# Optimization experiments

Measured on AMD Instinct MI355X. Metric: run time of the kernel, lower is better.

## Reference

```python
import jax, jax.numpy as jnp
import numpy as np

NUM_NODES = 100000
NUM_EDGES = 3200000
NUM_GRAPHS = 64


def gcn_conv(x, edge_index, W, b):
    """PyG GCNConv: add self-loops, symmetric deg normalization, linear, scatter-add."""
    n = x.shape[0]
    loop = jnp.arange(n, dtype=edge_index.dtype)
    src = jnp.concatenate([edge_index[0], loop])  # message sources
    dst = jnp.concatenate([edge_index[1], loop])  # aggregation targets
    deg = jax.ops.segment_sum(jnp.ones_like(src, dtype=x.dtype), dst, num_segments=n)
    dis = jnp.where(deg > 0, jax.lax.rsqrt(jnp.maximum(deg, 1.0)), 0.0)
    norm = dis[src] * dis[dst]  # [E+N]
    h = x @ W  # linear transform first (small dims)
    msg = h[src] * norm[:, None]  # irregular gather
    out = jax.ops.segment_sum(msg, dst, num_segments=n)  # scatter-add
    return out + b


def setup_inputs() -> dict:
    key = jax.random.key(0)
    ks = jax.random.split(key, 12)
    x = jax.random.normal(ks[0], (NUM_NODES, 3), dtype=jnp.float32)
    edge_index = jax.random.randint(ks[1], (2, NUM_EDGES), 0, NUM_NODES, dtype=jnp.int64)
    batch = jnp.sort(jax.random.randint(ks[2], (NUM_NODES,), 0, NUM_GRAPHS, dtype=jnp.int64))
    def glorot(k, fan_in, fan_out):
        s = (6.0 / (fan_in + fan_out)) ** 0.5
        return jax.random.uniform(k, (fan_in, fan_out), jnp.float32, -s, s)
    return {
        'x': x, 'edge_index': edge_index, 'batch': batch,
        'W1': glorot(ks[3], 3, 32), 'b1': jnp.zeros((32,), jnp.float32),
        'W2': glorot(ks[4], 32, 16), 'b2': jnp.zeros((16,), jnp.float32),
        'W3': glorot(ks[5], 16, 8), 'b3': jnp.zeros((8,), jnp.float32),
        'Wf': glorot(ks[6], 8, 3), 'bf': jnp.zeros((3,), jnp.float32),
    }


def reference(x, edge_index, batch, W1, b1, W2, b2, W3, b3, Wf, bf):
    h = jax.nn.relu(gcn_conv(x, edge_index, W1, b1))
    h = jax.nn.relu(gcn_conv(h, edge_index, W2, b2))
    h = jax.nn.relu(gcn_conv(h, edge_index, W3, b3))
    # global mean pool over graphs
    sums = jax.ops.segment_sum(h, batch, num_segments=NUM_GRAPHS)
    cnts = jax.ops.segment_sum(jnp.ones((h.shape[0],), h.dtype), batch, num_segments=NUM_GRAPHS)
    pooled = sums / jnp.maximum(cnts, 1.0)[:, None]
    return pooled @ Wf + bf
```

## Files before the change

### kernel.cpp

```cpp
#include <hip/hip_runtime.h>

constexpr int N_NODES  = 100000;
constexpr int N_EDGES  = 3200000;
constexpr int N_GRAPHS = 64;

constexpr int BSHIFT   = 8;
constexpr int NBINS    = (N_NODES + 255) >> BSHIFT;
constexpr int BIN_CAP  = 9216;
constexpr int SRC_BITS = 17;
constexpr int SRC_MASK = (1 << SRC_BITS) - 1;

constexpr int NB_BIN = 500;
constexpr int EPB    = N_EDGES / NB_BIN;
constexpr int EPT    = (EPB + 1023) / 1024;

typedef float v4f __attribute__((ext_vector_type(4)));


__global__ __launch_bounds__(1024) void bin_kernel(
        const int* __restrict__ src, const int* __restrict__ dst,
        int* __restrict__ bin_cur, int* __restrict__ binned) {
    __shared__ int pk[EPB];
    __shared__ unsigned short bn[EPB];
    __shared__ unsigned short ord[EPB];
    __shared__ int hist[NBINS];
    __shared__ int lexcl[NBINS];
    __shared__ int lofs[NBINS];
    __shared__ int gofs[NBINS];
    __shared__ int s512[512];
    int tid = threadIdx.x;
    int e0 = blockIdx.x * EPB;
    for (int i = tid; i < NBINS; i += 1024) hist[i] = 0;
    __syncthreads();
#pragma unroll
    for (int k = 0; k < EPT; ++k) {
        int i = tid + k * 1024;
        if (i < EPB) {
            int d = __builtin_nontemporal_load(&dst[e0 + i]);
            int s = __builtin_nontemporal_load(&src[e0 + i]);
            int b = d >> BSHIFT;
            pk[i] = ((d & 255) << SRC_BITS) | s;
            bn[i] = (unsigned short)b;
            atomicAdd(&hist[b], 1);
        }
    }
    __syncthreads();
    if (tid < 512) s512[tid] = (tid < NBINS) ? hist[tid] : 0;
    __syncthreads();
    for (int o = 1; o < 512; o <<= 1) {
        int x = 0;
        if (tid < 512 && tid >= o) x = s512[tid - o];
        __syncthreads();
        if (tid < 512) s512[tid] += x;
        __syncthreads();
    }
    if (tid < NBINS) {
        int h = hist[tid];
        int excl = s512[tid] - h;
        lexcl[tid] = excl;
        lofs[tid]  = excl;
        gofs[tid]  = h ? atomicAdd(&bin_cur[tid], h) : 0;
    }
    __syncthreads();
#pragma unroll
    for (int k = 0; k < EPT; ++k) {
        int i = tid + k * 1024;
        if (i < EPB) {
            int r = atomicAdd(&lofs[bn[i]], 1);
            ord[r] = (unsigned short)i;
        }
    }
    __syncthreads();
#pragma unroll
    for (int k = 0; k < EPT; ++k) {
        int i = tid + k * 1024;
        if (i < EPB) {
            int j = ord[i];
            int b = bn[j];
            int pos = gofs[b] + (i - lexcl[b]);
            if (pos < BIN_CAP)
                __builtin_nontemporal_store(pk[j], &binned[(size_t)b * BIN_CAP + pos]);
        }
    }
}

__global__ void binscan_kernel(const int* __restrict__ bin_cur, int* __restrict__ bin_base,
                               int* __restrict__ rowptr) {
    __shared__ int s[512];
    int t = threadIdx.x;
    int v = (t < NBINS) ? bin_cur[t] : 0;
    s[t] = v;
    __syncthreads();
    for (int o = 1; o < 512; o <<= 1) {
        int x = (t >= o) ? s[t - o] : 0;
        __syncthreads();
        s[t] += x;
        __syncthreads();
    }
    if (t < NBINS) bin_base[t] = s[t] - v;
    if (t == 0) rowptr[N_NODES] = N_EDGES;
}

__global__ __launch_bounds__(1024) void csrbuild_kernel(
        const int* __restrict__ binned, const int* __restrict__ bin_cur,
        const int* __restrict__ bin_base, int* __restrict__ rowptr,
        float* __restrict__ dis, int* __restrict__ csr) {
    __shared__ int cnt[256];
    __shared__ int lofs[256];
    __shared__ int s[256];
    int b = blockIdx.x;
    int t = threadIdx.x;
    int size  = min(bin_cur[b], BIN_CAP);
    int gbase = bin_base[b];
    const int* bp = binned + (size_t)b * BIN_CAP;
    if (t < 256) cnt[t] = 0;
    __syncthreads();
    int pc[9];
#pragma unroll
    for (int k = 0; k < 9; ++k) {
        int i = t + k * 1024;
        pc[k] = (i < size) ? __builtin_nontemporal_load(&bp[i]) : -1;
        if (i < size) atomicAdd(&cnt[pc[k] >> SRC_BITS], 1);
    }
    __syncthreads();
    if (t < 256) {
        int n = (b << BSHIFT) + t;
        int deg = cnt[t];
        if (n < N_NODES) dis[n] = 1.0f / sqrtf((float)deg + 1.0f);
        s[t] = deg;
    }
    __syncthreads();
    for (int o = 1; o < 256; o <<= 1) {
        int x = 0;
        if (t < 256 && t >= o) x = s[t - o];
        __syncthreads();
        if (t < 256) s[t] += x;
        __syncthreads();
    }
    if (t < 256) {
        int n = (b << BSHIFT) + t;
        int excl = s[t] - cnt[t];
        if (n < N_NODES) rowptr[n] = gbase + excl;
        lofs[t] = excl;
        cnt[t] = 0;
    }
    __syncthreads();
#pragma unroll
    for (int k = 0; k < 9; ++k) {
        int i = t + k * 1024;
        if (i < size) {
            int p = pc[k];
            int ln = p >> SRC_BITS;
            int r = atomicAdd(&cnt[ln], 1);
            csr[gbase + lofs[ln] + r] = p & SRC_MASK;
        }
    }
}


__global__ void pre1_kernel(const float* __restrict__ x, const float* __restrict__ dis,
                            float* __restrict__ xs) {
    int i = blockIdx.x * blockDim.x + threadIdx.x;
    if (i >= N_NODES) return;
    float d = dis[i];
    float4 v;
    v.x = __builtin_nontemporal_load(&x[(size_t)i * 3 + 0]) * d;
    v.y = __builtin_nontemporal_load(&x[(size_t)i * 3 + 1]) * d;
    v.z = __builtin_nontemporal_load(&x[(size_t)i * 3 + 2]) * d;
    v.w = 0.f;
    *reinterpret_cast<float4*>(&xs[(size_t)i * 4]) = v;
}

template<int F, bool ADD_B, bool RELU>
__global__ __launch_bounds__(256) void gather_kernel(
        const float* __restrict__ in, const int* __restrict__ rowptr,
        const int* __restrict__ csr, const float* __restrict__ dis,
        const float* __restrict__ b, float* __restrict__ out) {
    constexpr int VPL = F / 4;
    constexpr int NPB = 256 / 16;
    int tid  = threadIdx.x;
    int sub  = tid & 3;
    int qtr  = (tid >> 2) & 3;
    int n    = blockIdx.x * NPB + (tid >> 4);
    if (n >= N_NODES) return;
    int beg = rowptr[n], end = rowptr[n + 1];
    int len = end - beg;
    int kb = beg + ((len * qtr) >> 2);
    int ke = beg + ((len * (qtr + 1)) >> 2);
    const float* ip = in + (size_t)sub * VPL;
    float a0[VPL], a1[VPL], a2[VPL], a3[VPL];
#pragma unroll
    for (int j = 0; j < VPL; ++j) { a0[j] = 0.f; a1[j] = 0.f; a2[j] = 0.f; a3[j] = 0.f; }
    if (qtr == 0) {
#pragma unroll
        for (int j = 0; j < VPL; ++j) a0[j] = ip[(size_t)n * F + j];
    }
    int k = kb;
    for (; k + 7 < ke; k += 8) {
        int s0 = __builtin_nontemporal_load(&csr[k + 0]);
        int s1 = __builtin_nontemporal_load(&csr[k + 1]);
        int s2 = __builtin_nontemporal_load(&csr[k + 2]);
        int s3 = __builtin_nontemporal_load(&csr[k + 3]);
        int s4 = __builtin_nontemporal_load(&csr[k + 4]);
        int s5 = __builtin_nontemporal_load(&csr[k + 5]);
        int s6 = __builtin_nontemporal_load(&csr[k + 6]);
        int s7 = __builtin_nontemporal_load(&csr[k + 7]);
        const float* r0 = &ip[(size_t)s0 * F];
        const float* r1 = &ip[(size_t)s1 * F];
        const float* r2 = &ip[(size_t)s2 * F];
        const float* r3 = &ip[(size_t)s3 * F];
        const float* r4 = &ip[(size_t)s4 * F];
        const float* r5 = &ip[(size_t)s5 * F];
        const float* r6 = &ip[(size_t)s6 * F];
        const float* r7 = &ip[(size_t)s7 * F];
#pragma unroll
        for (int j = 0; j < VPL; ++j) a0[j] += r0[j];
#pragma unroll
        for (int j = 0; j < VPL; ++j) a1[j] += r1[j];
#pragma unroll
        for (int j = 0; j < VPL; ++j) a2[j] += r2[j];
#pragma unroll
        for (int j = 0; j < VPL; ++j) a3[j] += r3[j];
#pragma unroll
        for (int j = 0; j < VPL; ++j) a0[j] += r4[j];
#pragma unroll
        for (int j = 0; j < VPL; ++j) a1[j] += r5[j];
#pragma unroll
        for (int j = 0; j < VPL; ++j) a2[j] += r6[j];
#pragma unroll
        for (int j = 0; j < VPL; ++j) a3[j] += r7[j];
    }
    if (k + 3 < ke) {
        int s0 = __builtin_nontemporal_load(&csr[k + 0]);
        int s1 = __builtin_nontemporal_load(&csr[k + 1]);
        int s2 = __builtin_nontemporal_load(&csr[k + 2]);
        int s3 = __builtin_nontemporal_load(&csr[k + 3]);
        const float* r0 = &ip[(size_t)s0 * F];
        const float* r1 = &ip[(size_t)s1 * F];
        const float* r2 = &ip[(size_t)s2 * F];
        const float* r3 = &ip[(size_t)s3 * F];
#pragma unroll
        for (int j = 0; j < VPL; ++j) a0[j] += r0[j];
#pragma unroll
        for (int j = 0; j < VPL; ++j) a1[j] += r1[j];
#pragma unroll
        for (int j = 0; j < VPL; ++j) a2[j] += r2[j];
#pragma unroll
        for (int j = 0; j < VPL; ++j) a3[j] += r3[j];
        k += 4;
    }
    for (; k < ke; ++k) {
        int s0 = __builtin_nontemporal_load(&csr[k]);
        const float* r0 = &ip[(size_t)s0 * F];
#pragma unroll
        for (int j = 0; j < VPL; ++j) a0[j] += r0[j];
    }
    float v[VPL];
#pragma unroll
    for (int j = 0; j < VPL; ++j) v[j] = (a0[j] + a1[j]) + (a2[j] + a3[j]);
#pragma unroll
    for (int j = 0; j < VPL; ++j) v[j] += __shfl_xor(v[j], 4);
#pragma unroll
    for (int j = 0; j < VPL; ++j) v[j] += __shfl_xor(v[j], 8);
    if (qtr == 0) {
        float d = dis[n];
#pragma unroll
        for (int j = 0; j < VPL; ++j) {
            float w = v[j] * d;
            if (ADD_B) w += b[sub * VPL + j];
            if (RELU) w = fmaxf(w, 0.f);
            __builtin_nontemporal_store(w, &out[(size_t)n * F + sub * VPL + j]);
        }
    }
}

__global__ void lin1_kernel(const float* __restrict__ m, const float* __restrict__ W1,
                            const float* __restrict__ b1, float* __restrict__ h1) {
    int i = blockIdx.x * blockDim.x + threadIdx.x;
    if (i >= N_NODES) return;
    float4 mv = *reinterpret_cast<const float4*>(&m[(size_t)i * 4]);
#pragma unroll
    for (int f = 0; f < 32; ++f) {
        float s = b1[f];
        s = fmaf(mv.x, W1[0 * 32 + f], s);
        s = fmaf(mv.y, W1[1 * 32 + f], s);
        s = fmaf(mv.z, W1[2 * 32 + f], s);
        h1[(size_t)i * 32 + f] = fmaxf(s, 0.f);
    }
}

template<int FIN, int FOUT>
__global__ void lin_pre_kernel(const float* __restrict__ in, const float* __restrict__ W,
                               const float* __restrict__ dis, float* __restrict__ g) {
    int i = blockIdx.x * blockDim.x + threadIdx.x;
    if (i >= N_NODES) return;
    float xin[FIN];
    const v4f* hp = reinterpret_cast<const v4f*>(&in[(size_t)i * FIN]);
#pragma unroll
    for (int q = 0; q < FIN / 4; ++q) {
        v4f v = __builtin_nontemporal_load(&hp[q]);
        xin[q * 4 + 0] = v.x; xin[q * 4 + 1] = v.y;
        xin[q * 4 + 2] = v.z; xin[q * 4 + 3] = v.w;
    }
    float d = dis[i];
#pragma unroll
    for (int f = 0; f < FOUT; ++f) {
        float s = 0.f;
#pragma unroll
        for (int k = 0; k < FIN; ++k) s = fmaf(xin[k], W[k * FOUT + f], s);
        g[(size_t)i * FOUT + f] = s * d;
    }
}


__global__ void pool_kernel(const float* __restrict__ h, const int* __restrict__ batch,
                            float* __restrict__ pool) {
    __shared__ float lsum[N_GRAPHS * 8];
    __shared__ float lcnt[N_GRAPHS];
    int tid = threadIdx.x;
    for (int j = tid; j < N_GRAPHS * 8; j += blockDim.x) lsum[j] = 0.f;
    for (int j = tid; j < N_GRAPHS; j += blockDim.x) lcnt[j] = 0.f;
    __syncthreads();
    int i = blockIdx.x * blockDim.x + tid;
    if (i < N_NODES) {
        int gm = batch[i];
        const float4* hp = reinterpret_cast<const float4*>(&h[(size_t)i * 8]);
        float4 a = hp[0], bq = hp[1];
        atomicAdd(&lsum[gm * 8 + 0], a.x);
        atomicAdd(&lsum[gm * 8 + 1], a.y);
        atomicAdd(&lsum[gm * 8 + 2], a.z);
        atomicAdd(&lsum[gm * 8 + 3], a.w);
        atomicAdd(&lsum[gm * 8 + 4], bq.x);
        atomicAdd(&lsum[gm * 8 + 5], bq.y);
        atomicAdd(&lsum[gm * 8 + 6], bq.z);
        atomicAdd(&lsum[gm * 8 + 7], bq.w);
        atomicAdd(&lcnt[gm], 1.0f);
    }
    __syncthreads();
    for (int idx = tid; idx < N_GRAPHS * 9; idx += blockDim.x) {
        int gm = idx / 9, j = idx % 9;
        if (lcnt[gm] != 0.f) {
            if (j < 8) atomicAdd(&pool[gm * 8 + j], lsum[gm * 8 + j]);
            else       atomicAdd(&pool[512 + gm], lcnt[gm]);
        }
    }
}

__global__ void final_kernel(const float* __restrict__ pool, const float* __restrict__ Wf,
                             const float* __restrict__ bf, float* __restrict__ out) {
    int t = threadIdx.x;
    if (t >= N_GRAPHS * 3) return;
    int gm = t / 3, c = t % 3;
    float cnt = fmaxf(pool[512 + gm], 1.0f);
    float s = 0.f;
#pragma unroll
    for (int f = 0; f < 8; ++f) s = fmaf(pool[gm * 8 + f] / cnt, Wf[f * 3 + c], s);
    out[t] = s + bf[c];
}


extern "C" void kernel_launch(void* const* d_in, const int* in_sizes, int n_in,
                              void* d_out, int out_size, void* d_ws, size_t ws_size,
                              hipStream_t stream) {
    const float* x     = (const float*)d_in[0];
    const int*   ei    = (const int*)d_in[1];
    const int*   batch = (const int*)d_in[2];
    const float* W1 = (const float*)d_in[3];
    const float* b1 = (const float*)d_in[4];
    const float* W2 = (const float*)d_in[5];
    const float* b2 = (const float*)d_in[6];
    const float* W3 = (const float*)d_in[7];
    const float* b3 = (const float*)d_in[8];
    const float* Wf = (const float*)d_in[9];
    const float* bf = (const float*)d_in[10];

    const int* src = ei;
    const int* dst = ei + N_EDGES;

    const int N = N_NODES, E = N_EDGES;

    int*   bin_cur  = (int*)d_ws;
    int*   bin_base = bin_cur + NBINS;
    int*   rowptr   = bin_base + NBINS;
    float* dis      = (float*)(rowptr + N + 2);
    int*   csr      = (int*)(dis + N);
    float* act      = (float*)(csr + E);
    int*   binned   = (int*)act;
    float* xs   = act;
    float* m    = act + (size_t)4  * N;
    float* h1   = act + (size_t)8  * N;
    float* g    = act + (size_t)40 * N;
    float* h2   = act + (size_t)56 * N;
    float* pool = act + (size_t)72 * N;
    float* g8   = act;
    float* h3   = act + (size_t)8 * N;

    const int B = 256;
    const int NB_N = (N + B - 1) / B;
    const int NB_G = N / 16;

    hipMemsetAsync(bin_cur, 0, NBINS * sizeof(int), stream);
    hipMemsetAsync(pool, 0, N_GRAPHS * 9 * sizeof(float), stream);

    bin_kernel<<<NB_BIN, 1024, 0, stream>>>(src, dst, bin_cur, binned);
    binscan_kernel<<<1, 512, 0, stream>>>(bin_cur, bin_base, rowptr);
    csrbuild_kernel<<<NBINS, 1024, 0, stream>>>(binned, bin_cur, bin_base, rowptr, dis, csr);

    pre1_kernel<<<NB_N, B, 0, stream>>>(x, dis, xs);
    gather_kernel<4, false, false><<<NB_G, B, 0, stream>>>(xs, rowptr, csr, dis, b1, m);
    lin1_kernel<<<NB_N, B, 0, stream>>>(m, W1, b1, h1);

    lin_pre_kernel<32, 16><<<NB_N, B, 0, stream>>>(h1, W2, dis, g);
    gather_kernel<16, true, true><<<NB_G, B, 0, stream>>>(g, rowptr, csr, dis, b2, h2);

    lin_pre_kernel<16, 8><<<NB_N, B, 0, stream>>>(h2, W3, dis, g8);
    gather_kernel<8, true, true><<<NB_G, B, 0, stream>>>(g8, rowptr, csr, dis, b3, h3);

    pool_kernel<<<NB_N, B, 0, stream>>>(h3, batch, pool);
    final_kernel<<<1, 256, 0, stream>>>(pool, Wf, bf, (float*)d_out);
}
```

Baseline: 199.5 us.

## Fuse linear layers into gathers and pooling; split CSR rows by source half

Fuses lin1 with the W2 transform into one kernel, fuses the layer-2 gather with bias, ReLU and the W3 projection, and fuses the layer-3 gather with mean-pool accumulation. This removes three kernel launches and the round trips of the h1, h2 and h3 intermediates through global memory. The CSR build now sorts each row's edges into two halves by source index (below and above 50000) and records a rowmid pointer. The layer-2 gather walks the two halves separately, likely to improve cache locality of the gathered rows. The cost is extra shuffles, a larger scan in csrbuild, and more register pressure in the fused kernels.

```diff
diff --git a/kernel.cpp b/kernel.cpp
--- a/kernel.cpp
+++ b/kernel.cpp
@@ -3,6 +3,7 @@
 constexpr int N_NODES  = 100000;
 constexpr int N_EDGES  = 3200000;
 constexpr int N_GRAPHS = 64;
+constexpr int HALF_N   = 50000;
 
 constexpr int BSHIFT   = 8;
 constexpr int NBINS    = (N_NODES + 255) >> BSHIFT;
@@ -104,97 +105,70 @@
 __global__ __launch_bounds__(1024) void csrbuild_kernel(
         const int* __restrict__ binned, const int* __restrict__ bin_cur,
         const int* __restrict__ bin_base, int* __restrict__ rowptr,
-        float* __restrict__ dis, int* __restrict__ csr) {
-    __shared__ int cnt[256];
-    __shared__ int lofs[256];
-    __shared__ int s[256];
+        int* __restrict__ rowmid, float* __restrict__ dis, int* __restrict__ csr) {
+    __shared__ int cnt[512];
+    __shared__ int lofs[512];
+    __shared__ int s[512];
     int b = blockIdx.x;
     int t = threadIdx.x;
     int size  = min(bin_cur[b], BIN_CAP);
     int gbase = bin_base[b];
     const int* bp = binned + (size_t)b * BIN_CAP;
-    if (t < 256) cnt[t] = 0;
+    if (t < 512) cnt[t] = 0;
     __syncthreads();
     int pc[9];
 #pragma unroll
     for (int k = 0; k < 9; ++k) {
         int i = t + k * 1024;
         pc[k] = (i < size) ? __builtin_nontemporal_load(&bp[i]) : -1;
-        if (i < size) atomicAdd(&cnt[pc[k] >> SRC_BITS], 1);
-    }
+        if (i < size) {
+            int p = pc[k];
+            int idx = ((p >> SRC_BITS) << 1) | ((p & SRC_MASK) >= HALF_N);
+            atomicAdd(&cnt[idx], 1);
+        }
+    }
+    __syncthreads();
+    if (t < 512) s[t] = cnt[t];
+    __syncthreads();
+    for (int o = 1; o < 512; o <<= 1) {
+        int x = 0;
+        if (t < 512 && t >= o) x = s[t - o];
+        __syncthreads();
+        if (t < 512) s[t] += x;
+        __syncthreads();
+    }
+    if (t < 512) lofs[t] = s[t] - cnt[t];
     __syncthreads();
     if (t < 256) {
         int n = (b << BSHIFT) + t;
-        int deg = cnt[t];
-        if (n < N_NODES) dis[n] = 1.0f / sqrtf((float)deg + 1.0f);
-        s[t] = deg;
-    }
-    __syncthreads();
-    for (int o = 1; o < 256; o <<= 1) {
-        int x = 0;
-        if (t < 256 && t >= o) x = s[t - o];
-        __syncthreads();
-        if (t < 256) s[t] += x;
-        __syncthreads();
-    }
-    if (t < 256) {
-        int n = (b << BSHIFT) + t;
-        int excl = s[t] - cnt[t];
-        if (n < N_NODES) rowptr[n] = gbase + excl;
-        lofs[t] = excl;
-        cnt[t] = 0;
-    }
+        if (n < N_NODES) {
+            int deg = cnt[2 * t] + cnt[2 * t + 1];
+            dis[n] = 1.0f / sqrtf((float)deg + 1.0f);
+            rowptr[n] = gbase + lofs[2 * t];
+            rowmid[n] = gbase + lofs[2 * t + 1];
+        }
+    }
+    __syncthreads();
+    if (t < 512) cnt[t] = 0;
     __syncthreads();
 #pragma unroll
     for (int k = 0; k < 9; ++k) {
         int i = t + k * 1024;
         if (i < size) {
             int p = pc[k];
-            int ln = p >> SRC_BITS;
-            int r = atomicAdd(&cnt[ln], 1);
-            csr[gbase + lofs[ln] + r] = p & SRC_MASK;
-        }
-    }
-}
-
-
-__global__ void pre1_kernel(const float* __restrict__ x, const float* __restrict__ dis,
-                            float* __restrict__ xs) {
-    int i = blockIdx.x * blockDim.x + threadIdx.x;
-    if (i >= N_NODES) return;
-    float d = dis[i];
-    float4 v;
-    v.x = __builtin_nontemporal_load(&x[(size_t)i * 3 + 0]) * d;
-    v.y = __builtin_nontemporal_load(&x[(size_t)i * 3 + 1]) * d;
-    v.z = __builtin_nontemporal_load(&x[(size_t)i * 3 + 2]) * d;
-    v.w = 0.f;
-    *reinterpret_cast<float4*>(&xs[(size_t)i * 4]) = v;
-}
-
-template<int F, bool ADD_B, bool RELU>
-__global__ __launch_bounds__(256) void gather_kernel(
-        const float* __restrict__ in, const int* __restrict__ rowptr,
-        const int* __restrict__ csr, const float* __restrict__ dis,
-        const float* __restrict__ b, float* __restrict__ out) {
-    constexpr int VPL = F / 4;
-    constexpr int NPB = 256 / 16;
-    int tid  = threadIdx.x;
-    int sub  = tid & 3;
-    int qtr  = (tid >> 2) & 3;
-    int n    = blockIdx.x * NPB + (tid >> 4);
-    if (n >= N_NODES) return;
-    int beg = rowptr[n], end = rowptr[n + 1];
-    int len = end - beg;
-    int kb = beg + ((len * qtr) >> 2);
-    int ke = beg + ((len * (qtr + 1)) >> 2);
-    const float* ip = in + (size_t)sub * VPL;
-    float a0[VPL], a1[VPL], a2[VPL], a3[VPL];
-#pragma unroll
-    for (int j = 0; j < VPL; ++j) { a0[j] = 0.f; a1[j] = 0.f; a2[j] = 0.f; a3[j] = 0.f; }
-    if (qtr == 0) {
-#pragma unroll
-        for (int j = 0; j < VPL; ++j) a0[j] = ip[(size_t)n * F + j];
-    }
+            int srcv = p & SRC_MASK;
+            int idx = ((p >> SRC_BITS) << 1) | (srcv >= HALF_N);
+            int r = atomicAdd(&cnt[idx], 1);
+            csr[gbase + lofs[idx] + r] = srcv;
+        }
+    }
+}
+
+
+template<int F, int VPL>
+__device__ __forceinline__ void accum_range(
+        const float* __restrict__ ip, const int* __restrict__ csr, int kb, int ke,
+        float (&a0)[VPL], float (&a1)[VPL], float (&a2)[VPL], float (&a3)[VPL]) {
     int k = kb;
     for (; k + 7 < ke; k += 8) {
         int s0 = __builtin_nontemporal_load(&csr[k + 0]);
@@ -255,89 +229,169 @@
 #pragma unroll
         for (int j = 0; j < VPL; ++j) a0[j] += r0[j];
     }
-    float v[VPL];
-#pragma unroll
-    for (int j = 0; j < VPL; ++j) v[j] = (a0[j] + a1[j]) + (a2[j] + a3[j]);
-#pragma unroll
-    for (int j = 0; j < VPL; ++j) v[j] += __shfl_xor(v[j], 4);
-#pragma unroll
-    for (int j = 0; j < VPL; ++j) v[j] += __shfl_xor(v[j], 8);
-    if (qtr == 0) {
-        float d = dis[n];
-#pragma unroll
-        for (int j = 0; j < VPL; ++j) {
-            float w = v[j] * d;
-            if (ADD_B) w += b[sub * VPL + j];
-            if (RELU) w = fmaxf(w, 0.f);
-            __builtin_nontemporal_store(w, &out[(size_t)n * F + sub * VPL + j]);
-        }
-    }
-}
-
-__global__ void lin1_kernel(const float* __restrict__ m, const float* __restrict__ W1,
-                            const float* __restrict__ b1, float* __restrict__ h1) {
+}
+
+
+__global__ void pre1_kernel(const float* __restrict__ x, const float* __restrict__ dis,
+                            float* __restrict__ xs) {
     int i = blockIdx.x * blockDim.x + threadIdx.x;
     if (i >= N_NODES) return;
+    float d = dis[i];
+    float4 v;
+    v.x = __builtin_nontemporal_load(&x[(size_t)i * 3 + 0]) * d;
+    v.y = __builtin_nontemporal_load(&x[(size_t)i * 3 + 1]) * d;
+    v.z = __builtin_nontemporal_load(&x[(size_t)i * 3 + 2]) * d;
+    v.w = 0.f;
+    *reinterpret_cast<float4*>(&xs[(size_t)i * 4]) = v;
+}
+
+__global__ __launch_bounds__(256) void gather4_kernel(
+        const float* __restrict__ in, const int* __restrict__ rowptr,
+        const int* __restrict__ csr, const float* __restrict__ dis,
+        float* __restrict__ out) {
+    constexpr int F = 4, VPL = 1;
+    int tid = threadIdx.x;
+    int sub = tid & 3, qtr = (tid >> 2) & 3;
+    int n = blockIdx.x * 16 + (tid >> 4);
+    int beg = rowptr[n], end = rowptr[n + 1];
+    int len = end - beg;
+    const float* ip = in + sub;
+    float a0[1], a1[1], a2[1], a3[1];
+    a0[0] = (qtr == 0) ? ip[(size_t)n * F] : 0.f;
+    a1[0] = 0.f; a2[0] = 0.f; a3[0] = 0.f;
+    accum_range<F, VPL>(ip, csr, beg + ((len * qtr) >> 2), beg + ((len * (qtr + 1)) >> 2),
+                        a0, a1, a2, a3);
+    float v = (a0[0] + a1[0]) + (a2[0] + a3[0]);
+    v += __shfl_xor(v, 4);
+    v += __shfl_xor(v, 8);
+    if (qtr == 0)
+        __builtin_nontemporal_store(v * dis[n], &out[(size_t)n * F + sub]);
+}
+
+__global__ __launch_bounds__(256) void linfuse_kernel(
+        const float* __restrict__ m, const float* __restrict__ W1,
+        const float* __restrict__ b1, const float* __restrict__ W2,
+        const float* __restrict__ dis, float* __restrict__ g) {
+    __shared__ float w2s[512];
+    __shared__ float w1s[96];
+    __shared__ float b1s[32];
+    int tid = threadIdx.x;
+    for (int j = tid; j < 512; j += 256) w2s[j] = W2[j];
+    if (tid < 96) w1s[tid] = W1[tid];
+    if (tid < 32) b1s[tid] = b1[tid];
+    __syncthreads();
+    int i = blockIdx.x * blockDim.x + tid;
+    if (i >= N_NODES) return;
     float4 mv = *reinterpret_cast<const float4*>(&m[(size_t)i * 4]);
+    float h[32];
 #pragma unroll
     for (int f = 0; f < 32; ++f) {
-        float s = b1[f];
-        s = fmaf(mv.x, W1[0 * 32 + f], s);
-        s = fmaf(mv.y, W1[1 * 32 + f], s);
-        s = fmaf(mv.z, W1[2 * 32 + f], s);
-        h1[(size_t)i * 32 + f] = fmaxf(s, 0.f);
-    }
-}
-
-template<int FIN, int FOUT>
-__global__ void lin_pre_kernel(const float* __restrict__ in, const float* __restrict__ W,
-                               const float* __restrict__ dis, float* __restrict__ g) {
-    int i = blockIdx.x * blockDim.x + threadIdx.x;
-    if (i >= N_NODES) return;
-    float xin[FIN];
-    const v4f* hp = reinterpret_cast<const v4f*>(&in[(size_t)i * FIN]);
-#pragma unroll
-    for (int q = 0; q < FIN / 4; ++q) {
-        v4f v = __builtin_nontemporal_load(&hp[q]);
-        xin[q * 4 + 0] = v.x; xin[q * 4 + 1] = v.y;
-        xin[q * 4 + 2] = v.z; xin[q * 4 + 3] = v.w;
+        float s = b1s[f];
+        s = fmaf(mv.x, w1s[f], s);
+        s = fmaf(mv.y, w1s[32 + f], s);
+        s = fmaf(mv.z, w1s[64 + f], s);
+        h[f] = fmaxf(s, 0.f);
     }
     float d = dis[i];
 #pragma unroll
-    for (int f = 0; f < FOUT; ++f) {
+    for (int o = 0; o < 16; ++o) {
         float s = 0.f;
 #pragma unroll
-        for (int k = 0; k < FIN; ++k) s = fmaf(xin[k], W[k * FOUT + f], s);
-        g[(size_t)i * FOUT + f] = s * d;
-    }
-}
-
-
-__global__ void pool_kernel(const float* __restrict__ h, const int* __restrict__ batch,
-                            float* __restrict__ pool) {
+        for (int f = 0; f < 32; ++f) s = fmaf(h[f], w2s[f * 16 + o], s);
+        g[(size_t)i * 16 + o] = s * d;
+    }
+}
+
+__global__ __launch_bounds__(256) void gather16w3_kernel(
+        const float* __restrict__ in, const int* __restrict__ rowptr,
+        const int* __restrict__ rowmid, const int* __restrict__ csr,
+        const float* __restrict__ dis, const float* __restrict__ b2,
+        const float* __restrict__ W3, float* __restrict__ g8) {
+    __shared__ float w3s[128];
+    int tid = threadIdx.x;
+    if (tid < 128) w3s[tid] = W3[tid];
+    __syncthreads();
+    constexpr int F = 16, VPL = 4;
+    int sub = tid & 3, qtr = (tid >> 2) & 3;
+    int n = blockIdx.x * 16 + (tid >> 4);
+    int beg = rowptr[n], mid = rowmid[n], end = rowptr[n + 1];
+    int lenA = mid - beg, lenB = end - mid;
+    const float* ip = in + (size_t)sub * VPL;
+    float a0[4], a1[4], a2[4], a3[4];
+#pragma unroll
+    for (int j = 0; j < 4; ++j) { a1[j] = 0.f; a2[j] = 0.f; a3[j] = 0.f; }
+#pragma unroll
+    for (int j = 0; j < 4; ++j) a0[j] = (qtr == 0) ? ip[(size_t)n * F + j] : 0.f;
+    accum_range<F, VPL>(ip, csr, beg + ((lenA * qtr) >> 2), beg + ((lenA * (qtr + 1)) >> 2),
+                        a0, a1, a2, a3);
+    accum_range<F, VPL>(ip, csr, mid + ((lenB * qtr) >> 2), mid + ((lenB * (qtr + 1)) >> 2),
+                        a0, a1, a2, a3);
+    float d = dis[n];
+    float w[4];
+#pragma unroll
+    for (int j = 0; j < 4; ++j) {
+        float v = (a0[j] + a1[j]) + (a2[j] + a3[j]);
+        v += __shfl_xor(v, 4);
+        v += __shfl_xor(v, 8);
+        w[j] = fmaxf(fmaf(v, d, b2[sub * 4 + j]), 0.f);
+    }
+    float p[8];
+#pragma unroll
+    for (int o = 0; o < 8; ++o) {
+        float s = 0.f;
+#pragma unroll
+        for (int j = 0; j < 4; ++j) s = fmaf(w[j], w3s[(sub * 4 + j) * 8 + o], s);
+        s += __shfl_xor(s, 1);
+        s += __shfl_xor(s, 2);
+        p[o] = s;
+    }
+    if (qtr == 0) {
+        g8[(size_t)n * 8 + sub * 2 + 0] = p[sub * 2 + 0] * d;
+        g8[(size_t)n * 8 + sub * 2 + 1] = p[sub * 2 + 1] * d;
+    }
+}
+
+__global__ __launch_bounds__(256) void gather8pool_kernel(
+        const float* __restrict__ in, const int* __restrict__ rowptr,
+        const int* __restrict__ csr, const float* __restrict__ dis,
+        const float* __restrict__ b3, const int* __restrict__ batch,
+        float* __restrict__ pool) {
     __shared__ float lsum[N_GRAPHS * 8];
     __shared__ float lcnt[N_GRAPHS];
     int tid = threadIdx.x;
-    for (int j = tid; j < N_GRAPHS * 8; j += blockDim.x) lsum[j] = 0.f;
-    for (int j = tid; j < N_GRAPHS; j += blockDim.x) lcnt[j] = 0.f;
-    __syncthreads();
-    int i = blockIdx.x * blockDim.x + tid;
-    if (i < N_NODES) {
-        int gm = batch[i];
-        const float4* hp = reinterpret_cast<const float4*>(&h[(size_t)i * 8]);
-        float4 a = hp[0], bq = hp[1];
-        atomicAdd(&lsum[gm * 8 + 0], a.x);
-        atomicAdd(&lsum[gm * 8 + 1], a.y);
-        atomicAdd(&lsum[gm * 8 + 2], a.z);
-        atomicAdd(&lsum[gm * 8 + 3], a.w);
-        atomicAdd(&lsum[gm * 8 + 4], bq.x);
-        atomicAdd(&lsum[gm * 8 + 5], bq.y);
-        atomicAdd(&lsum[gm * 8 + 6], bq.z);
-        atomicAdd(&lsum[gm * 8 + 7], bq.w);
-        atomicAdd(&lcnt[gm], 1.0f);
-    }
-    __syncthreads();
-    for (int idx = tid; idx < N_GRAPHS * 9; idx += blockDim.x) {
+    for (int j = tid; j < N_GRAPHS * 8; j += 256) lsum[j] = 0.f;
+    if (tid < N_GRAPHS) lcnt[tid] = 0.f;
+    __syncthreads();
+    constexpr int F = 8, VPL = 2;
+    int sub = tid & 3, qtr = (tid >> 2) & 3;
+    int n = blockIdx.x * 16 + (tid >> 4);
+    int beg = rowptr[n], end = rowptr[n + 1];
+    int len = end - beg;
+    const float* ip = in + (size_t)sub * VPL;
+    float a0[2], a1[2], a2[2], a3[2];
+#pragma unroll
+    for (int j = 0; j < 2; ++j) { a1[j] = 0.f; a2[j] = 0.f; a3[j] = 0.f; }
+#pragma unroll
+    for (int j = 0; j < 2; ++j) a0[j] = (qtr == 0) ? ip[(size_t)n * F + j] : 0.f;
+    accum_range<F, VPL>(ip, csr, beg + ((len * qtr) >> 2), beg + ((len * (qtr + 1)) >> 2),
+                        a0, a1, a2, a3);
+    float d = dis[n];
+    if (true) {
+#pragma unroll
+        for (int j = 0; j < 2; ++j) {
+            float v = (a0[j] + a1[j]) + (a2[j] + a3[j]);
+            v += __shfl_xor(v, 4);
+            v += __shfl_xor(v, 8);
+            if (qtr == 0) {
+                float h = fmaxf(fmaf(v, d, b3[sub * 2 + j]), 0.f);
+                int gm = batch[n];
+                atomicAdd(&lsum[gm * 8 + sub * 2 + j], h);
+                if (sub == 0 && j == 0) atomicAdd(&lcnt[gm], 1.0f);
+            }
+        }
+    }
+    __syncthreads();
+    for (int idx = tid; idx < N_GRAPHS * 9; idx += 256) {
         int gm = idx / 9, j = idx % 9;
         if (lcnt[gm] != 0.f) {
             if (j < 8) atomicAdd(&pool[gm * 8 + j], lsum[gm * 8 + j]);
@@ -377,23 +431,21 @@
     const int* src = ei;
     const int* dst = ei + N_EDGES;
 
-    const int N = N_NODES, E = N_EDGES;
+    const int N = N_NODES;
 
     int*   bin_cur  = (int*)d_ws;
     int*   bin_base = bin_cur + NBINS;
     int*   rowptr   = bin_base + NBINS;
-    float* dis      = (float*)(rowptr + N + 2);
+    int*   rowmid   = rowptr + (N + 2);
+    float* dis      = (float*)(rowmid + N);
     int*   csr      = (int*)(dis + N);
-    float* act      = (float*)(csr + E);
+    float* act      = (float*)(csr + N_EDGES);
     int*   binned   = (int*)act;
     float* xs   = act;
     float* m    = act + (size_t)4  * N;
-    float* h1   = act + (size_t)8  * N;
-    float* g    = act + (size_t)40 * N;
-    float* h2   = act + (size_t)56 * N;
-    float* pool = act + (size_t)72 * N;
-    float* g8   = act;
-    float* h3   = act + (size_t)8 * N;
+    float* g    = act + (size_t)8  * N;
+    float* g8   = act + (size_t)24 * N;
+    float* pool = act + (size_t)36 * N;
 
     const int B = 256;
     const int NB_N = (N + B - 1) / B;
@@ -404,18 +456,15 @@
 
     bin_kernel<<<NB_BIN, 1024, 0, stream>>>(src, dst, bin_cur, binned);
     binscan_kernel<<<1, 512, 0, stream>>>(bin_cur, bin_base, rowptr);
-    csrbuild_kernel<<<NBINS, 1024, 0, stream>>>(binned, bin_cur, bin_base, rowptr, dis, csr);
+    csrbuild_kernel<<<NBINS, 1024, 0, stream>>>(binned, bin_cur, bin_base, rowptr, rowmid, dis, csr);
 
     pre1_kernel<<<NB_N, B, 0, stream>>>(x, dis, xs);
-    gather_kernel<4, false, false><<<NB_G, B, 0, stream>>>(xs, rowptr, csr, dis, b1, m);
-    lin1_kernel<<<NB_N, B, 0, stream>>>(m, W1, b1, h1);
-
-    lin_pre_kernel<32, 16><<<NB_N, B, 0, stream>>>(h1, W2, dis, g);
-    gather_kernel<16, true, true><<<NB_G, B, 0, stream>>>(g, rowptr, csr, dis, b2, h2);
-
-    lin_pre_kernel<16, 8><<<NB_N, B, 0, stream>>>(h2, W3, dis, g8);
-    gather_kernel<8, true, true><<<NB_G, B, 0, stream>>>(g8, rowptr, csr, dis, b3, h3);
-
-    pool_kernel<<<NB_N, B, 0, stream>>>(h3, batch, pool);
+    gather4_kernel<<<NB_G, B, 0, stream>>>(xs, rowptr, csr, dis, m);
+    linfuse_kernel<<<NB_N, B, 0, stream>>>(m, W1, b1, W2, dis, g);
+
+    gather16w3_kernel<<<NB_G, B, 0, stream>>>(g, rowptr, rowmid, csr, dis, b2, W3, g8);
+
+    gather8pool_kernel<<<NB_G, B, 0, stream>>>(g8, rowptr, csr, dis, b3, batch, pool);
+
     final_kernel<<<1, 256, 0, stream>>>(pool, Wf, bf, (float*)d_out);
 }
```

After: 219.4 us. 1.1x slower.
